# Optimization experiments

Hardware: AMD Instinct MI355X
Metric: run time of the kernel (lower is better)

## Reference

```python
import jax, jax.numpy as jnp
import numpy as np


def setup_inputs() -> dict:
    key = jax.random.key(0)
    ks = jax.random.split(key, 10)
    B, C, H, W = 4, 64, 96, 96
    C8 = C // 8
    R = C // 16  # CBAM reduction ratio 16
    s = 0.05
    return {
        "x": jax.random.normal(ks[0], (B, C, H, W), dtype=jnp.float32),
        "wq": jax.random.normal(ks[1], (C8, C), dtype=jnp.float32) * s,
        "bq": jnp.zeros((C8,), dtype=jnp.float32),
        "wk": jax.random.normal(ks[2], (C8, C), dtype=jnp.float32) * s,
        "bk": jnp.zeros((C8,), dtype=jnp.float32),
        "wv": jax.random.normal(ks[3], (C, C), dtype=jnp.float32) * s,
        "bv": jnp.zeros((C,), dtype=jnp.float32),
        "ca_w1": jax.random.normal(ks[4], (R, C), dtype=jnp.float32) * s,
        "ca_w2": jax.random.normal(ks[5], (C, R), dtype=jnp.float32) * s,
    }


def reference(x, wq, bq, wk, bk, wv, bv, ca_w1, ca_w2):
    B, C, H, W = x.shape
    N = H * W
    # 1x1 convs as channel einsums
    q = jnp.einsum('bchw,oc->bohw', x, wq) + bq[None, :, None, None]  # [B,C/8,H,W]
    k = jnp.einsum('bchw,oc->bohw', x, wk) + bk[None, :, None, None]
    v = jnp.einsum('bchw,oc->bohw', x, wv) + bv[None, :, None, None]  # [B,C,H,W]
    Q = q.reshape(B, -1, N)          # [B,C8,N]
    K = k.reshape(B, -1, N)          # [B,C8,N]
    V = v.reshape(B, C, N)           # [B,C,N]
    energy = jnp.einsum('bcn,bcm->bnm', Q, K)   # [B,N,N] = Q^T K
    att = jax.nn.sigmoid(energy)
    # out = V @ att^T  -> out[b,c,n] = sum_m V[b,c,m] * att[b,n,m]
    out = jnp.einsum('bcm,bnm->bcn', V, att).reshape(B, C, H, W)
    out = out + x
    # CBAM channel attention: shared bias-free MLP on avg & max pooled features
    avg = out.mean(axis=(2, 3))      # [B,C]
    mx = out.max(axis=(2, 3))        # [B,C]
    def mlp(f):
        h = jax.nn.relu(jnp.einsum('bc,rc->br', f, ca_w1))
        return jnp.einsum('br,cr->bc', h, ca_w2)
    scale = jax.nn.sigmoid(mlp(avg) + mlp(mx))  # [B,C]
    return out * scale[:, :, None, None]
```

## Files before the change

kernel.cpp:

```cpp
#include <hip/hip_runtime.h>
#include <hip/hip_bf16.h>

#define B_  4
#define C_  64
#define C8_ 8
#define N_  9216
#define NEG_LOG2E (-1.44269504088896340736f)

typedef _Float16 half8  __attribute__((ext_vector_type(8)));
typedef float    f32x16 __attribute__((ext_vector_type(16)));

static __device__ __forceinline__ float fast_exp2(float x){ float r; asm("v_exp_f32 %0, %1":"=v"(r):"v"(x)); return r; }
static __device__ __forceinline__ float fast_rcp (float x){ float r; asm("v_rcp_f32 %0, %1":"=v"(r):"v"(x)); return r; }

static __device__ __forceinline__ void gload16(const void* g, void* l){
    __builtin_amdgcn_global_load_lds((const __attribute__((address_space(1))) void*)g,
                                     (__attribute__((address_space(3))) void*)l, 16, 0, 0);
}

__global__ void qkv_kernel(const float* __restrict__ x,
                           const float* __restrict__ wq, const float* __restrict__ bq,
                           const float* __restrict__ wk, const float* __restrict__ bk,
                           const float* __restrict__ wv, const float* __restrict__ bv,
                           _Float16* __restrict__ Qt, _Float16* __restrict__ Kt,
                           _Float16* __restrict__ Vp) {
    __shared__ float xl[C_ * 128];
    __shared__ float wl[80 * C_];
    __shared__ float bl[80];
    const int bi = blockIdx.y;
    const int n0 = blockIdx.x * 128;
    const int tid = threadIdx.x;

    for (int i = tid; i < C_ * 128; i += 256) {
        int c = i >> 7, n = i & 127;
        xl[i] = x[(size_t)(bi * C_ + c) * N_ + n0 + n];
    }
    for (int i = tid; i < 80 * C_; i += 256) {
        wl[i] = (i < 512) ? wq[i] : (i < 1024) ? wk[i - 512] : wv[i - 1024];
    }
    if (tid < 80) bl[tid] = (tid < 8) ? bq[tid] : (tid < 16) ? bk[tid - 8] : bv[tid - 16];
    __syncthreads();

    const int n = tid & 127;
    const int g = tid >> 7;
    const int nn = n0 + n;
    const int low = nn & 15;
    const int g2 = (low >> 2) & 3;
    const int low2 = (g2 == 1) ? low + 4 : (g2 == 2) ? low - 4 : low;
    const int posn = (nn & ~15) | low2;

    for (int k = 0; k < 40; k += 4) {
        const int o = g * 40 + k;
        float a0 = bl[o], a1 = bl[o + 1], a2 = bl[o + 2], a3 = bl[o + 3];
        #pragma unroll 16
        for (int c = 0; c < C_; ++c) {
            float xv = xl[c * 128 + n];
            a0 += xv * wl[(o + 0) * C_ + c];
            a1 += xv * wl[(o + 1) * C_ + c];
            a2 += xv * wl[(o + 2) * C_ + c];
            a3 += xv * wl[(o + 3) * C_ + c];
        }
        if (o < 8) {
            _Float16* dst = Qt + ((size_t)(bi * N_) + nn) * 8 + o;
            dst[0] = (_Float16)(a0 * NEG_LOG2E); dst[1] = (_Float16)(a1 * NEG_LOG2E);
            dst[2] = (_Float16)(a2 * NEG_LOG2E); dst[3] = (_Float16)(a3 * NEG_LOG2E);
        } else if (o < 16) {
            _Float16* dst = Kt + ((size_t)(bi * N_) + nn) * 8 + (o - 8);
            dst[0] = (_Float16)a0; dst[1] = (_Float16)a1;
            dst[2] = (_Float16)a2; dst[3] = (_Float16)a3;
        } else {
            const int c0 = o - 16;
            Vp[(size_t)(bi * C_ + c0 + 0) * N_ + posn] = (_Float16)a0;
            Vp[(size_t)(bi * C_ + c0 + 1) * N_ + posn] = (_Float16)a1;
            Vp[(size_t)(bi * C_ + c0 + 2) * N_ + posn] = (_Float16)a2;
            Vp[(size_t)(bi * C_ + c0 + 3) * N_ + posn] = (_Float16)a3;
        }
    }
}

#define VOFF 0
#define KOFF 16384
#define QOFF 18432
#define ZOFF 20480
#define LDSBYTES 20608

#define STAGE(mt, bsel) do {                                                            \
    const int m0s_ = mbase + (mt) * 64;                                                 \
    if (wave == 0)                                                                      \
        gload16(Kt + ((size_t)(b * N_ + m0s_) + lane) * 8, lds + KOFF + (bsel) * 1024); \
    {                                                                                   \
        const int ld0_ = wave * 2;                                                      \
        const int cl0_ = ld0_ * 8 + (lane >> 3);                                        \
        const int q0_  = (lane & 7) ^ (cl0_ & 7);                                       \
        gload16(Vp + (size_t)(b * C_ + cl0_) * N_ + m0s_ + q0_ * 8,                     \
                lds + VOFF + (bsel) * 8192 + ld0_ * 1024);                              \
        const int cl1_ = cl0_ + 8;                                                      \
        const int q1_  = (lane & 7) ^ (cl1_ & 7);                                       \
        gload16(Vp + (size_t)(b * C_ + cl1_) * N_ + m0s_ + q1_ * 8,                     \
                lds + VOFF + (bsel) * 8192 + (ld0_ + 1) * 1024);                        \
    } } while (0)

__global__ __launch_bounds__(256) void attn_kernel(
        const _Float16* __restrict__ Qt, const _Float16* __restrict__ Kt,
        const _Float16* __restrict__ Vp, float* __restrict__ part) {
    __shared__ ulong2 ldsq[LDSBYTES / 16];
    char* lds = (char*)ldsq;
    const int tid  = threadIdx.x;
    const int wave = tid >> 6, lane = tid & 63;
    const int l31  = lane & 31;
    const int hi   = lane >> 5;
    const int b    = blockIdx.z, mh = blockIdx.y;
    const int n0   = blockIdx.x * 128;
    const int mbase = mh * (N_ / 2);

    if (tid < 8) ((short*)(lds + ZOFF))[tid] = 0;

    STAGE(0, 0);
    if (wave == 1) {
        gload16(Qt + ((size_t)(b * N_ + n0) + lane) * 8,      lds + QOFF);
        gload16(Qt + ((size_t)(b * N_ + n0 + 64) + lane) * 8, lds + QOFF + 1024);
    }
    __syncthreads();

    const int qa = (lane < 32) ? (QOFF + (wave * 32 + l31) * 16) : ZOFF;
    const half8 qf = *(const half8*)(lds + qa);

    f32x16 acc0 = (f32x16)(0.f), acc1 = (f32x16)(0.f);

    for (int t = 0; t < 72; ++t) {
        const int buf = t & 1;
        if (t + 1 < 72) STAGE(t + 1, buf ^ 1);

        const int ka0 = (lane < 32) ? (KOFF + buf * 1024 +       l31 * 16) : ZOFF;
        const int ka1 = (lane < 32) ? (KOFF + buf * 1024 + 512 + l31 * 16) : ZOFF;
        const half8 kf0 = *(const half8*)(lds + ka0);
        const half8 kf1 = *(const half8*)(lds + ka1);
        f32x16 s0 = __builtin_amdgcn_mfma_f32_32x32x16_f16(kf0, qf, (f32x16)(0.f), 0, 0, 0);
        f32x16 s1 = __builtin_amdgcn_mfma_f32_32x32x16_f16(kf1, qf, (f32x16)(0.f), 0, 0, 0);

        #pragma unroll
        for (int r = 0; r < 16; ++r) s0[r] = fast_rcp(1.f + fast_exp2(s0[r]));
        #pragma unroll
        for (int r = 0; r < 16; ++r) s1[r] = fast_rcp(1.f + fast_exp2(s1[r]));

        const int vbase = VOFF + buf * 8192;
        #pragma unroll
        for (int ks = 0; ks < 4; ++ks) {
            f32x16 am = (ks < 2) ? s0 : s1;
            const int bb = (ks & 1) * 8;
            uint4 pk;
            pk.x = __builtin_bit_cast(unsigned int, __builtin_amdgcn_cvt_pkrtz(am[bb + 0], am[bb + 1]));
            pk.y = __builtin_bit_cast(unsigned int, __builtin_amdgcn_cvt_pkrtz(am[bb + 2], am[bb + 3]));
            pk.z = __builtin_bit_cast(unsigned int, __builtin_amdgcn_cvt_pkrtz(am[bb + 4], am[bb + 5]));
            pk.w = __builtin_bit_cast(unsigned int, __builtin_amdgcn_cvt_pkrtz(am[bb + 6], am[bb + 7]));
            const half8 bf = __builtin_bit_cast(half8, pk);
            const int sw = ((2 * ks + hi) ^ (l31 & 7)) * 16;
            const half8 af0 = *(const half8*)(lds + vbase + l31 * 128 + sw);
            const half8 af1 = *(const half8*)(lds + vbase + (32 + l31) * 128 + sw);
            acc0 = __builtin_amdgcn_mfma_f32_32x32x16_f16(af0, bf, acc0, 0, 0, 0);
            acc1 = __builtin_amdgcn_mfma_f32_32x32x16_f16(af1, bf, acc1, 0, 0, 0);
        }
        __syncthreads();
    }

    float* pp = part + ((size_t)(mh * B_ + b) * C_) * (size_t)N_ + n0 + wave * 32 + l31;
    #pragma unroll
    for (int r = 0; r < 16; ++r) {
        const int c0 = (r & 3) + 8 * (r >> 2) + 4 * hi;
        pp[(size_t)c0 * N_]        = acc0[r];
        pp[(size_t)(c0 + 32) * N_] = acc1[r];
    }
}

__global__ void reduce_pool(const float* __restrict__ part, const float* __restrict__ x,
                            float* __restrict__ outp,
                            float* __restrict__ avgP, float* __restrict__ maxP) {
    const int c = blockIdx.x, b = blockIdx.y;
    const size_t off = (size_t)(b * C_ + c) * N_;
    const float4* p0 = (const float4*)(part + ((size_t)(0 * B_ + b) * C_ + c) * N_);
    const float4* p1 = (const float4*)(part + ((size_t)(1 * B_ + b) * C_ + c) * N_);
    const float4* xr = (const float4*)(x + off);
    float4* orow = (float4*)(outp + off);
    const int tid = threadIdx.x;
    float s = 0.f, mx = -3.4e38f;
    for (int i = tid; i < N_ / 4; i += 256) {
        float4 a = p0[i], bq = p1[i], xv = xr[i];
        float4 o;
        o.x = a.x + bq.x + xv.x; o.y = a.y + bq.y + xv.y;
        o.z = a.z + bq.z + xv.z; o.w = a.w + bq.w + xv.w;
        orow[i] = o;
        s += o.x + o.y + o.z + o.w;
        mx = fmaxf(mx, fmaxf(fmaxf(o.x, o.y), fmaxf(o.z, o.w)));
    }
    #pragma unroll
    for (int offm = 32; offm > 0; offm >>= 1) {
        s += __shfl_down(s, offm, 64);
        mx = fmaxf(mx, __shfl_down(mx, offm, 64));
    }
    __shared__ float ss[4], sm[4];
    if ((tid & 63) == 0) { ss[tid >> 6] = s; sm[tid >> 6] = mx; }
    __syncthreads();
    if (tid == 0) {
        float fs = ss[0] + ss[1] + ss[2] + ss[3];
        float fm = fmaxf(fmaxf(sm[0], sm[1]), fmaxf(sm[2], sm[3]));
        avgP[b * C_ + c] = fs / (float)N_;
        maxP[b * C_ + c] = fm;
    }
}

__global__ void mlp_kernel(const float* __restrict__ avgP, const float* __restrict__ maxP,
                           const float* __restrict__ w1, const float* __restrict__ w2,
                           float* __restrict__ scaleP) {
    __shared__ float h[32];
    const int tid = threadIdx.x;
    if (tid < 32) {
        int b = tid >> 3, r = (tid >> 1) & 3, wh = tid & 1;
        const float* src = wh ? maxP : avgP;
        float s = 0.f;
        for (int c = 0; c < C_; ++c) s += src[b * C_ + c] * w1[r * C_ + c];
        h[tid] = fmaxf(s, 0.f);
    }
    __syncthreads();
    int b = tid >> 6, c = tid & 63;
    float s = 0.f;
    #pragma unroll
    for (int r = 0; r < 4; ++r)
        s += (h[b * 8 + r * 2] + h[b * 8 + r * 2 + 1]) * w2[c * 4 + r];
    scaleP[tid] = fast_rcp(1.f + fast_exp2(s * NEG_LOG2E));
}

__global__ void scale_kernel(float* __restrict__ outp, const float* __restrict__ scaleP) {
    int i4 = blockIdx.x * 256 + threadIdx.x;
    float sc = scaleP[i4 / (N_ / 4)];
    float4 v = *(const float4*)&outp[(size_t)i4 * 4];
    v.x *= sc; v.y *= sc; v.z *= sc; v.w *= sc;
    *(float4*)&outp[(size_t)i4 * 4] = v;
}

extern "C" void kernel_launch(void* const* d_in, const int* in_sizes, int n_in,
                              void* d_out, int out_size, void* d_ws, size_t ws_size,
                              hipStream_t stream) {
    const float* x  = (const float*)d_in[0];
    const float* wq = (const float*)d_in[1];
    const float* bq = (const float*)d_in[2];
    const float* wk = (const float*)d_in[3];
    const float* bk = (const float*)d_in[4];
    const float* wv = (const float*)d_in[5];
    const float* bv = (const float*)d_in[6];
    const float* w1 = (const float*)d_in[7];
    const float* w2 = (const float*)d_in[8];
    float* outp = (float*)d_out;

    char* w = (char*)d_ws;
    _Float16* Qt = (_Float16*)(w);
    _Float16* Kt = (_Float16*)(w + 589824);
    _Float16* Vp = (_Float16*)(w + 1179648);
    float* part  = (float*)(w + 5898240);
    float* avgP  = (float*)(w + 24772608);
    float* maxP  = avgP + 256;
    float* scaleP = maxP + 256;

    qkv_kernel<<<dim3(N_ / 128, B_), 256, 0, stream>>>(x, wq, bq, wk, bk, wv, bv, Qt, Kt, Vp);
    attn_kernel<<<dim3(N_ / 128, 2, B_), 256, 0, stream>>>(Qt, Kt, Vp, part);
    reduce_pool<<<dim3(C_, B_), 256, 0, stream>>>(part, x, outp, avgP, maxP);
    mlp_kernel<<<1, 256, 0, stream>>>(avgP, maxP, w1, w2, scaleP);
    scale_kernel<<<(B_ * C_ * N_ / 4) / 256, 256, 0, stream>>>(outp, scaleP);
}
```

Baseline: 239.6 us.

## Split attention key range four ways and compute QKV projection with MFMA

The attention kernel now splits the key/value dimension into four chunks instead of two, so the grid has twice as many blocks, each running a shorter loop. The reduce kernel sums four partial buffers instead of two. The QKV projection is rewritten to use f16 MFMA instructions in place of scalar fp32 FMAs from shared memory. The aim is better CU occupancy in the main attention kernel and a cheaper projection, at the cost of twice the partial-sum write and read traffic and fp16 rounding of x and the weights before the projection.

```diff
diff --git a/kernel.cpp b/kernel.cpp
--- a/kernel.cpp
+++ b/kernel.cpp
@@ -5,6 +5,11 @@
 #define C_  64
 #define C8_ 8
 #define N_  9216
+#define BN  128
+#define BM  64
+#define MSPLIT 4
+#define MCHUNK (N_ / MSPLIT)
+#define NITER  (MCHUNK / BM)
 #define NEG_LOG2E (-1.44269504088896340736f)
 
 typedef _Float16 half8  __attribute__((ext_vector_type(8)));
@@ -18,62 +23,68 @@
                                      (__attribute__((address_space(3))) void*)l, 16, 0, 0);
 }
 
-__global__ void qkv_kernel(const float* __restrict__ x,
-                           const float* __restrict__ wq, const float* __restrict__ bq,
-                           const float* __restrict__ wk, const float* __restrict__ bk,
-                           const float* __restrict__ wv, const float* __restrict__ bv,
-                           _Float16* __restrict__ Qt, _Float16* __restrict__ Kt,
-                           _Float16* __restrict__ Vp) {
-    __shared__ float xl[C_ * 128];
-    __shared__ float wl[80 * C_];
-    __shared__ float bl[80];
-    const int bi = blockIdx.y;
-    const int n0 = blockIdx.x * 128;
+__global__ __launch_bounds__(256) void qkv2_kernel(
+        const float* __restrict__ x,
+        const float* __restrict__ wq, const float* __restrict__ bq,
+        const float* __restrict__ wk, const float* __restrict__ bk,
+        const float* __restrict__ wv, const float* __restrict__ bv,
+        _Float16* __restrict__ Qt, _Float16* __restrict__ Kt,
+        _Float16* __restrict__ Vp) {
     const int tid = threadIdx.x;
-
-    for (int i = tid; i < C_ * 128; i += 256) {
-        int c = i >> 7, n = i & 127;
-        xl[i] = x[(size_t)(bi * C_ + c) * N_ + n0 + n];
-    }
-    for (int i = tid; i < 80 * C_; i += 256) {
-        wl[i] = (i < 512) ? wq[i] : (i < 1024) ? wk[i - 512] : wv[i - 1024];
-    }
-    if (tid < 80) bl[tid] = (tid < 8) ? bq[tid] : (tid < 16) ? bk[tid - 8] : bv[tid - 16];
-    __syncthreads();
-
-    const int n = tid & 127;
-    const int g = tid >> 7;
-    const int nn = n0 + n;
-    const int low = nn & 15;
+    const int wv_i = tid >> 6, lane = tid & 63, l31 = lane & 31, hi = lane >> 5;
+    const int b = blockIdx.y;
+    const int n = blockIdx.x * 128 + wv_i * 32 + l31;
+
+    half8 af[3][4];
+    #pragma unroll
+    for (int mt = 0; mt < 3; ++mt) {
+        const int o = mt * 32 + l31;
+        #pragma unroll
+        for (int kk = 0; kk < 4; ++kk) {
+            half8 a;
+            #pragma unroll
+            for (int j = 0; j < 8; ++j) {
+                const int c = kk * 16 + hi * 8 + j;
+                float v = 0.f;
+                if (o < 8)       v = wq[o * C_ + c] * NEG_LOG2E;
+                else if (o < 16) v = wk[(o - 8) * C_ + c];
+                else if (o < 80) v = wv[(o - 16) * C_ + c];
+                a[j] = (_Float16)v;
+            }
+            af[mt][kk] = a;
+        }
+    }
+    half8 bf[4];
+    #pragma unroll
+    for (int kk = 0; kk < 4; ++kk) {
+        half8 t;
+        #pragma unroll
+        for (int j = 0; j < 8; ++j) {
+            const int c = kk * 16 + hi * 8 + j;
+            t[j] = (_Float16)x[(size_t)(b * C_ + c) * N_ + n];
+        }
+        bf[kk] = t;
+    }
+    const int low = n & 15;
     const int g2 = (low >> 2) & 3;
     const int low2 = (g2 == 1) ? low + 4 : (g2 == 2) ? low - 4 : low;
-    const int posn = (nn & ~15) | low2;
-
-    for (int k = 0; k < 40; k += 4) {
-        const int o = g * 40 + k;
-        float a0 = bl[o], a1 = bl[o + 1], a2 = bl[o + 2], a3 = bl[o + 3];
-        #pragma unroll 16
-        for (int c = 0; c < C_; ++c) {
-            float xv = xl[c * 128 + n];
-            a0 += xv * wl[(o + 0) * C_ + c];
-            a1 += xv * wl[(o + 1) * C_ + c];
-            a2 += xv * wl[(o + 2) * C_ + c];
-            a3 += xv * wl[(o + 3) * C_ + c];
-        }
-        if (o < 8) {
-            _Float16* dst = Qt + ((size_t)(bi * N_) + nn) * 8 + o;
-            dst[0] = (_Float16)(a0 * NEG_LOG2E); dst[1] = (_Float16)(a1 * NEG_LOG2E);
-            dst[2] = (_Float16)(a2 * NEG_LOG2E); dst[3] = (_Float16)(a3 * NEG_LOG2E);
-        } else if (o < 16) {
-            _Float16* dst = Kt + ((size_t)(bi * N_) + nn) * 8 + (o - 8);
-            dst[0] = (_Float16)a0; dst[1] = (_Float16)a1;
-            dst[2] = (_Float16)a2; dst[3] = (_Float16)a3;
-        } else {
-            const int c0 = o - 16;
-            Vp[(size_t)(bi * C_ + c0 + 0) * N_ + posn] = (_Float16)a0;
-            Vp[(size_t)(bi * C_ + c0 + 1) * N_ + posn] = (_Float16)a1;
-            Vp[(size_t)(bi * C_ + c0 + 2) * N_ + posn] = (_Float16)a2;
-            Vp[(size_t)(bi * C_ + c0 + 3) * N_ + posn] = (_Float16)a3;
+    const int posn = (n & ~15) | low2;
+
+    #pragma unroll
+    for (int mt = 0; mt < 3; ++mt) {
+        f32x16 acc = (f32x16)(0.f);
+        #pragma unroll
+        for (int kk = 0; kk < 4; ++kk)
+            acc = __builtin_amdgcn_mfma_f32_32x32x16_f16(af[mt][kk], bf[kk], acc, 0, 0, 0);
+        #pragma unroll
+        for (int r = 0; r < 16; ++r) {
+            const int o = mt * 32 + (r & 3) + 8 * (r >> 2) + 4 * hi;
+            if (o < 8)
+                Qt[((size_t)(b * N_) + n) * 8 + o] = (_Float16)(acc[r] + bq[o] * NEG_LOG2E);
+            else if (o < 16)
+                Kt[((size_t)(b * N_) + n) * 8 + (o - 8)] = (_Float16)(acc[r] + bk[o - 8]);
+            else if (o < 80)
+                Vp[(size_t)(b * C_ + (o - 16)) * N_ + posn] = (_Float16)(acc[r] + bv[o - 16]);
         }
     }
 }
@@ -111,7 +122,7 @@
     const int hi   = lane >> 5;
     const int b    = blockIdx.z, mh = blockIdx.y;
     const int n0   = blockIdx.x * 128;
-    const int mbase = mh * (N_ / 2);
+    const int mbase = mh * MCHUNK;
 
     if (tid < 8) ((short*)(lds + ZOFF))[tid] = 0;
 
@@ -127,9 +138,9 @@
 
     f32x16 acc0 = (f32x16)(0.f), acc1 = (f32x16)(0.f);
 
-    for (int t = 0; t < 72; ++t) {
+    for (int t = 0; t < NITER; ++t) {
         const int buf = t & 1;
-        if (t + 1 < 72) STAGE(t + 1, buf ^ 1);
+        if (t + 1 < NITER) STAGE(t + 1, buf ^ 1);
 
         const int ka0 = (lane < 32) ? (KOFF + buf * 1024 +       l31 * 16) : ZOFF;
         const int ka1 = (lane < 32) ? (KOFF + buf * 1024 + 512 + l31 * 16) : ZOFF;
@@ -179,15 +190,19 @@
     const size_t off = (size_t)(b * C_ + c) * N_;
     const float4* p0 = (const float4*)(part + ((size_t)(0 * B_ + b) * C_ + c) * N_);
     const float4* p1 = (const float4*)(part + ((size_t)(1 * B_ + b) * C_ + c) * N_);
+    const float4* p2 = (const float4*)(part + ((size_t)(2 * B_ + b) * C_ + c) * N_);
+    const float4* p3 = (const float4*)(part + ((size_t)(3 * B_ + b) * C_ + c) * N_);
     const float4* xr = (const float4*)(x + off);
     float4* orow = (float4*)(outp + off);
     const int tid = threadIdx.x;
     float s = 0.f, mx = -3.4e38f;
     for (int i = tid; i < N_ / 4; i += 256) {
-        float4 a = p0[i], bq = p1[i], xv = xr[i];
+        float4 a = p0[i], bq = p1[i], cq = p2[i], dq = p3[i], xv = xr[i];
         float4 o;
-        o.x = a.x + bq.x + xv.x; o.y = a.y + bq.y + xv.y;
-        o.z = a.z + bq.z + xv.z; o.w = a.w + bq.w + xv.w;
+        o.x = a.x + bq.x + cq.x + dq.x + xv.x;
+        o.y = a.y + bq.y + cq.y + dq.y + xv.y;
+        o.z = a.z + bq.z + cq.z + dq.z + xv.z;
+        o.w = a.w + bq.w + cq.w + dq.w + xv.w;
         orow[i] = o;
         s += o.x + o.y + o.z + o.w;
         mx = fmaxf(mx, fmaxf(fmaxf(o.x, o.y), fmaxf(o.z, o.w)));
@@ -256,12 +271,12 @@
     _Float16* Kt = (_Float16*)(w + 589824);
     _Float16* Vp = (_Float16*)(w + 1179648);
     float* part  = (float*)(w + 5898240);
-    float* avgP  = (float*)(w + 24772608);
+    float* avgP  = (float*)(w + 43646976);
     float* maxP  = avgP + 256;
     float* scaleP = maxP + 256;
 
-    qkv_kernel<<<dim3(N_ / 128, B_), 256, 0, stream>>>(x, wq, bq, wk, bk, wv, bv, Qt, Kt, Vp);
-    attn_kernel<<<dim3(N_ / 128, 2, B_), 256, 0, stream>>>(Qt, Kt, Vp, part);
+    qkv2_kernel<<<dim3(N_ / 128, B_), 256, 0, stream>>>(x, wq, bq, wk, bk, wv, bv, Qt, Kt, Vp);
+    attn_kernel<<<dim3(N_ / 128, MSPLIT, B_), 256, 0, stream>>>(Qt, Kt, Vp, part);
     reduce_pool<<<dim3(C_, B_), 256, 0, stream>>>(part, x, outp, avgP, maxP);
     mlp_kernel<<<1, 256, 0, stream>>>(avgP, maxP, w1, w2, scaleP);
     scale_kernel<<<(B_ * C_ * N_ / 4) / 256, 256, 0, stream>>>(outp, scaleP);
```

New measurement: 210.7 us. 1.14x faster.
